# Optimization experiments

Hardware: AMD Instinct MI355X
Metric: run time of the kernel (lower is better)

Reference implementation:

```python
import jax, jax.numpy as jnp
import numpy as np

B, T, E, H, DEPTH = 128, 256, 512, 1024, 3


def setup_inputs() -> dict:
    key = jax.random.key(0)
    ks = jax.random.split(key, 9)
    s_e = 1.0 / np.sqrt(E)
    s_h = 1.0 / np.sqrt(H)
    return {
        "x": jax.random.normal(ks[0], (B, T, E), jnp.float32),
        "W_ih0": jax.random.normal(ks[1], (4 * H, E), jnp.float32) * s_e,
        "W_hh0": jax.random.normal(ks[2], (4 * H, H), jnp.float32) * s_h,
        "b_ih0": jax.random.normal(ks[3], (4 * H,), jnp.float32) * s_h,
        "b_hh0": jax.random.normal(ks[4], (4 * H,), jnp.float32) * s_h,
        "W_ih_r": jax.random.normal(ks[5], (DEPTH - 1, 4 * H, H), jnp.float32) * s_h,
        "W_hh_r": jax.random.normal(ks[6], (DEPTH - 1, 4 * H, H), jnp.float32) * s_h,
        "b_ih_r": jax.random.normal(ks[7], (DEPTH - 1, 4 * H), jnp.float32) * s_h,
        "b_hh_r": jax.random.normal(ks[8], (DEPTH - 1, 4 * H), jnp.float32) * s_h,
        "trainable": 1,
    }


def _lstm_cell(inp, h, c, Wih, Whh, bih, bhh):
    # torch.nn.LSTMCell: gates = inp @ Wih.T + bih + h @ Whh.T + bhh; order i,f,g,o
    gates = inp @ Wih.T + bih + h @ Whh.T + bhh
    i, f, g, o = jnp.split(gates, 4, axis=-1)
    c_new = jax.nn.sigmoid(f) * c + jax.nn.sigmoid(i) * jnp.tanh(g)
    h_new = jax.nn.sigmoid(o) * jnp.tanh(c_new)
    return h_new, c_new


def reference(x, W_ih0, W_hh0, b_ih0, b_hh0, W_ih_r, W_hh_r, b_ih_r, b_hh_r, trainable):
    b, _, _ = x.shape
    h_dim = W_hh0.shape[1]
    n_rest = W_ih_r.shape[0]
    zeros = jnp.zeros((b, h_dim), x.dtype)
    x_t = jnp.swapaxes(x, 0, 1)  # [T, B, E]

    def step(carry, xt):
        hs, cs = carry  # each [n_rest, B, H]
        # faithful bug: layer-0 state is never updated -> always zeros
        h, c = _lstm_cell(xt, zeros, zeros, W_ih0, W_hh0, b_ih0, b_hh0)
        new_h, new_c = [], []
        for l in range(n_rest):  # small fixed depth loop
            h, c = _lstm_cell(h, hs[l], cs[l], W_ih_r[l], W_hh_r[l], b_ih_r[l], b_hh_r[l])
            new_h.append(h)
            new_c.append(c)
        return (jnp.stack(new_h), jnp.stack(new_c)), h

    init = (jnp.zeros((n_rest, b, h_dim), x.dtype),
            jnp.zeros((n_rest, b, h_dim), x.dtype))
    _, out = jax.lax.scan(step, init, x_t)
    return out  # [T, B, H] == list of top-layer h per timestep
```

## Files before the change

### kernel.cpp

```cpp
#include <hip/hip_runtime.h>

static constexpr int Bc = 128;
static constexpr int Tc = 256;
static constexpr int Ec = 512;
static constexpr int Hc = 1024;
static constexpr int SLOT = Bc * Hc;

using bf16x8 = __attribute__((ext_vector_type(8))) short;
using f32x4  = __attribute__((ext_vector_type(4))) float;

__device__ __forceinline__ unsigned short f2bf(float f) {
  unsigned int u = __float_as_uint(f);
  u += 0x7FFFu + ((u >> 16) & 1u);
  return (unsigned short)(u >> 16);
}
__device__ __forceinline__ float sigm(float x) { return 1.0f / (1.0f + __expf(-x)); }
__device__ __forceinline__ float ftanh(float x) { return 1.0f - 2.0f / (__expf(2.0f * x) + 1.0f); }

#define MFMA16(A, Bf, C) __builtin_amdgcn_mfma_f32_16x16x32_bf16((A), (Bf), (C), 0, 0, 0)

__device__ __forceinline__ void poll_rlx(const int* p, int tgt) {
  while (__hip_atomic_load(p, __ATOMIC_RELAXED, __HIP_MEMORY_SCOPE_AGENT) < tgt)
    __builtin_amdgcn_s_sleep(1);
}
__device__ __forceinline__ void sig(int* p, int v) {
  __hip_atomic_store(p, v, __ATOMIC_RELAXED, __HIP_MEMORY_SCOPE_AGENT);
}
__device__ __forceinline__ void stg_c(unsigned short* p, unsigned short v) {
  __hip_atomic_store(p, v, __ATOMIC_RELAXED, __HIP_MEMORY_SCOPE_AGENT);
}
__device__ __forceinline__ int lds_acq(const int* p) {
  return __hip_atomic_load(p, __ATOMIC_ACQUIRE, __HIP_MEMORY_SCOPE_WORKGROUP);
}
__device__ __forceinline__ void lds_rel(int* p, int v) {
  __hip_atomic_store(p, v, __ATOMIC_RELEASE, __HIP_MEMORY_SCOPE_WORKGROUP);
}

__global__ void k_cvt_bf16(const float* __restrict__ src, unsigned short* __restrict__ dst, int n) {
  int i = (blockIdx.x * blockDim.x + threadIdx.x) * 4;
  if (i + 3 < n) {
    f32x4 v = *(const f32x4*)(src + i);
    *(ushort4*)(dst + i) = make_ushort4(f2bf(v[0]), f2bf(v[1]), f2bf(v[2]), f2bf(v[3]));
  }
}

__global__ void k_prep_small(const float* __restrict__ bih0, const float* __restrict__ bhh0,
                             float* __restrict__ b0s,
                             unsigned short* __restrict__ h2c,
                             int* __restrict__ f1, int* __restrict__ f2) {
  int i = blockIdx.x * blockDim.x + threadIdx.x;
  if (i < 4096) b0s[i] = bih0[i] + bhh0[i];
  h2c[i] = 0;
  if (i < 128 * 16) { f1[i] = 0; f2[i] = 0; }
}

__global__ __launch_bounds__(256, 1) void k_l0(
    const unsigned short* __restrict__ xb, const unsigned short* __restrict__ W0,
    const float* __restrict__ b0s, unsigned short* __restrict__ H0)
{
  __shared__ unsigned short Axs[64 * 128 * 8];
  const int tid = threadIdx.x;
  const int lane = tid & 63, wid = tid >> 6;
  const int bx = blockIdx.x;
  const int jbase = blockIdx.y * 64 + wid * 16;
  const int ri = lane & 15, kg = lane >> 4;

  for (int i = tid; i < 8192; i += 256) {
    const int row = i >> 6;
    const int chunk = i & 63;
    const int phys = chunk * 128 + (row ^ (chunk & 15));
    *(bf16x8*)(Axs + (size_t)phys * 8) =
        *(const bf16x8*)(xb + ((size_t)row * Tc + bx) * Ec + chunk * 8);
  }
  __syncthreads();

  const int j = jbase + ri;
  const float bi = b0s[j], bg = b0s[2 * Hc + j], bo = b0s[3 * Hc + j];
  const unsigned short* w0r = W0 + ((size_t)(0 * Hc + j)) * Ec + kg * 8;
  const unsigned short* w2r = W0 + ((size_t)(2 * Hc + j)) * Ec + kg * 8;
  const unsigned short* w3r = W0 + ((size_t)(3 * Hc + j)) * Ec + kg * 8;

  f32x4 ai[8], ag[8], ao[8];
#pragma unroll
  for (int u = 0; u < 8; ++u) { ai[u] = (f32x4){0,0,0,0}; ag[u] = (f32x4){0,0,0,0}; ao[u] = (f32x4){0,0,0,0}; }

#pragma unroll 4
  for (int kk = 0; kk < Ec / 32; ++kk) {
    bf16x8 wi = *(const bf16x8*)(w0r + kk * 32);
    bf16x8 wg = *(const bf16x8*)(w2r + kk * 32);
    bf16x8 wo = *(const bf16x8*)(w3r + kk * 32);
    const int ch = kk * 4 + kg;
#pragma unroll
    for (int u = 0; u < 8; ++u) {
      const int phys = ch * 128 + ((u * 16 + ri) ^ (ch & 15));
      bf16x8 a = *(const bf16x8*)(Axs + (size_t)phys * 8);
      ai[u] = MFMA16(a, wi, ai[u]);
      ag[u] = MFMA16(a, wg, ag[u]);
      ao[u] = MFMA16(a, wo, ao[u]);
    }
  }

  unsigned short* hb = H0 + (size_t)bx * SLOT + (size_t)(j >> 3) * 1024 + (j & 7);
#pragma unroll
  for (int u = 0; u < 8; ++u) {
#pragma unroll
    for (int q = 0; q < 4; ++q) {
      const int b = u * 16 + kg * 4 + q;
      float c = sigm(ai[u][q] + bi) * ftanh(ag[u][q] + bg);
      float h = sigm(ao[u][q] + bo) * ftanh(c);
      hb[(size_t)b * 8] = f2bf(h);
    }
  }
}

__global__ __launch_bounds__(512, 1) void k_rec(
    const unsigned short* H0,
    const float* __restrict__ Wih, const float* __restrict__ Whh,
    const float* __restrict__ bih, const float* __restrict__ bhh,
    unsigned short* h1c,
    unsigned short* h2c,
    int* f1, int* f2,
    float* out)
{
  __shared__ unsigned short Wlds[2 * 64 * 64 * 8];
  __shared__ float pbuf[4][4][64][4];
  __shared__ int flg[32];
  int* sF_   = flg + 0;
  int* sG_   = flg + 4;
  int* pollD = flg + 8;
  int* pollF = flg + 12;
  int* doneS = flg + 16;

  const int tid = threadIdx.x;
  const int lane = tid & 63, wid = tid >> 6;
  const int m = wid & 3;
  const bool gatedw = (wid >= 4);
  const int bid = blockIdx.x;
  const int layer = bid >> 7;
  const int w = bid & 127;
  const int j0 = w * 8;
  const int ri = lane & 15, kg = lane >> 4;

  if (tid < 32) flg[tid] = 0;

  const size_t lw = (size_t)layer * 4096 * 1024;
  for (int s = tid; s < 2 * 64 * 64; s += 512) {
    const int l   = s & 63;
    const int kkg = (s >> 6) & 63;
    const int t   = s >> 12;
    const int rr  = l & 15;
    const int gate = t * 2 + (rr >> 3);
    const int R = gate * 1024 + j0 + (rr & 7);
    const int k = kkg * 32 + (l >> 4) * 8;
    const float* src = (k < 1024) ? (Wih + lw + (size_t)R * 1024 + k)
                                  : (Whh + lw + (size_t)R * 1024 + (k - 1024));
    f32x4 v0 = *(const f32x4*)src;
    f32x4 v1 = *(const f32x4*)(src + 4);
    ushort4* d = (ushort4*)(Wlds + (size_t)s * 8);
    d[0] = make_ushort4(f2bf(v0[0]), f2bf(v0[1]), f2bf(v0[2]), f2bf(v0[3]));
    d[1] = make_ushort4(f2bf(v1[0]), f2bf(v1[1]), f2bf(v1[2]), f2bf(v1[3]));
  }

  const int jme = j0 + (ri & 7);
  const int g0 = (ri < 8) ? 0 : 1;
  const int g1 = (ri < 8) ? 2 : 3;
  const float bias0 = bih[layer * 4096 + g0 * 1024 + jme] + bhh[layer * 4096 + g0 * 1024 + jme];
  const float bias1 = bih[layer * 4096 + g1 * 1024 + jme] + bhh[layer * 4096 + g1 * 1024 + jme];

  float c0[4]  = {0.f, 0.f, 0.f, 0.f};
  float c1s[4] = {0.f, 0.f, 0.f, 0.f};

  const unsigned short* lds0 = Wlds + (size_t)lane * 8;
  const unsigned short* lds1 = Wlds + (size_t)64 * 64 * 8 + (size_t)lane * 8;
  const int abase = kg * 1024 + (m * 32 + ri) * 8;
  const bool lo = (ri < 8);

  f32x4 acc00, acc01, acc10, acc11;
#define ZERO4() { acc00 = (f32x4){0,0,0,0}; acc01 = (f32x4){0,0,0,0}; \
                  acc10 = (f32x4){0,0,0,0}; acc11 = (f32x4){0,0,0,0}; }
#define PLOAD()  { acc00 = *(const f32x4*)&pbuf[m][0][lane][0]; \
                   acc01 = *(const f32x4*)&pbuf[m][1][lane][0]; \
                   acc10 = *(const f32x4*)&pbuf[m][2][lane][0]; \
                   acc11 = *(const f32x4*)&pbuf[m][3][lane][0]; }
#define PWRITE() { *(f32x4*)&pbuf[m][0][lane][0] = acc00; \
                   *(f32x4*)&pbuf[m][1][lane][0] = acc01; \
                   *(f32x4*)&pbuf[m][2][lane][0] = acc10; \
                   *(f32x4*)&pbuf[m][3][lane][0] = acc11; }

#define HALF_MM4(Abase, LDSOFF)                                             \
  {                                                                         \
    const unsigned short* ap_ = (Abase) + abase;                            \
    _Pragma("unroll")                                                       \
    for (int kk = 0; kk < 32; ++kk) {                                       \
      bf16x8 b0 = *(const bf16x8*)(lds0 + (LDSOFF) + kk * 512);             \
      bf16x8 b1 = *(const bf16x8*)(lds1 + (LDSOFF) + kk * 512);             \
      bf16x8 vlo = *(const bf16x8*)(ap_ + kk * 4096);                       \
      bf16x8 vhi = *(const bf16x8*)(ap_ + kk * 4096 + 128);                 \
      acc00 = MFMA16(vlo, b0, acc00);                                       \
      acc01 = MFMA16(vlo, b1, acc01);                                       \
      acc10 = MFMA16(vhi, b0, acc10);                                       \
      acc11 = MFMA16(vhi, b1, acc11);                                       \
    }                                                                       \
  }

#define CELL4(accA, accB, cre, hnarr)                                       \
  _Pragma("unroll")                                                         \
  for (int q = 0; q < 4; ++q) {                                             \
    float x0 = accA[q] + bias0;                                             \
    float x1 = accB[q] + bias1;                                             \
    float p0 = __shfl_xor(x0, 8);                                           \
    float p1 = __shfl_xor(x1, 8);                                           \
    float gi = lo ? x0 : p0;                                                \
    float gf = lo ? p0 : x0;                                                \
    float gg = lo ? x1 : p1;                                                \
    float go = lo ? p1 : x1;                                                \
    float cn = sigm(gf) * cre[q] + sigm(gi) * ftanh(gg);                    \
    hnarr[q] = sigm(go) * ftanh(cn);                                        \
    cre[q] = cn;                                                            \
  }

#define GPOLL_BAR(farr, tgt, stamp)                                         \
  { if (lane < 32) poll_rlx((farr) + (m * 32 + lane) * 16, (tgt));          \
    if (lane == 0) lds_rel(&(stamp)[m], (tgt));                             \
    while (lds_acq(&(stamp)[0]) < (tgt) || lds_acq(&(stamp)[1]) < (tgt) ||  \
           lds_acq(&(stamp)[2]) < (tgt) || lds_acq(&(stamp)[3]) < (tgt)) {} }

  __syncthreads();

  if (layer == 0) {
    if (!gatedw) {
      ZERO4() HALF_MM4(H0, 0)
      for (int t = 0; t < Tc; ++t) {
        while (lds_acq(&sG_[m]) < t) {}
        PWRITE()
        if (lane == 0) lds_rel(&sF_[m], t + 1);
        if (t + 1 < Tc) { ZERO4() HALF_MM4(H0 + (size_t)(t + 1) * SLOT, 0) }
      }
    } else {
      for (int p = 0; p < Tc; ++p) {
        if (p >= 1) GPOLL_BAR(f1, p, pollD)
        while (lds_acq(&sF_[m]) < p + 1) {}
        PLOAD()
        if (lane == 0) lds_rel(&sG_[m], p + 1);
        if (p >= 1) HALF_MM4(h1c + (size_t)(p - 1) * SLOT, 32 * 512)
        float hn0[4], hn1[4];
        CELL4(acc00, acc01, c0, hn0)
        CELL4(acc10, acc11, c1s, hn1)
        if (lo) {
          unsigned short* hb = h1c + (size_t)p * SLOT + (size_t)w * 1024 + (ri & 7);
#pragma unroll
          for (int q = 0; q < 4; ++q) {
            const int r0 = m * 32 + kg * 4 + q;
            stg_c(hb + (size_t)r0 * 8, f2bf(hn0[q]));
            stg_c(hb + (size_t)(r0 + 16) * 8, f2bf(hn1[q]));
          }
        }
        __asm__ volatile("s_waitcnt vmcnt(0)" ::: "memory");
        if (lane == 0) lds_rel(&doneS[m], p + 1);
        if (m == 0) {
          while (lds_acq(&doneS[1]) < p + 1 || lds_acq(&doneS[2]) < p + 1 ||
                 lds_acq(&doneS[3]) < p + 1) {}
          if (lane == 0) sig(f1 + w * 16, p + 1);
        }
      }
    }
  } else {
    if (!gatedw) {
      GPOLL_BAR(f1, 1, pollF)
      ZERO4() HALF_MM4(h1c, 0)
      for (int t = 0; t < Tc; ++t) {
        while (lds_acq(&sG_[m]) < t) {}
        PWRITE()
        if (lane == 0) lds_rel(&sF_[m], t + 1);
        if (t + 1 < Tc) {
          GPOLL_BAR(f1, t + 2, pollF)
          ZERO4() HALF_MM4(h1c + (size_t)(t + 1) * SLOT, 0)
        }
      }
    } else {
      for (int s = 0; s < Tc; ++s) {
        if (s >= 1) GPOLL_BAR(f2, s, pollD)
        __builtin_amdgcn_fence(__ATOMIC_ACQUIRE, "agent");
        while (lds_acq(&sF_[m]) < s + 1) {}
        PLOAD()
        if (lane == 0) lds_rel(&sG_[m], s + 1);
        HALF_MM4(h2c + (size_t)((s - 1) & 3) * SLOT, 32 * 512)
        float hn0[4], hn1[4];
        CELL4(acc00, acc01, c0, hn0)
        CELL4(acc10, acc11, c1s, hn1)
        if (lo) {
          unsigned short* hb = h2c + (size_t)(s & 3) * SLOT + (size_t)w * 1024 + (ri & 7);
#pragma unroll
          for (int q = 0; q < 4; ++q) {
            const int r0 = m * 32 + kg * 4 + q;
            stg_c(hb + (size_t)r0 * 8, f2bf(hn0[q]));
            stg_c(hb + (size_t)(r0 + 16) * 8, f2bf(hn1[q]));
          }
        }
        __asm__ volatile("s_waitcnt vmcnt(0)" ::: "memory");
        if (lane == 0) lds_rel(&doneS[m], s + 1);
        if (m == 0) {
          while (lds_acq(&doneS[1]) < s + 1 || lds_acq(&doneS[2]) < s + 1 ||
                 lds_acq(&doneS[3]) < s + 1) {}
          if (lane == 0) sig(f2 + w * 16, s + 1);
        }
        if (lo) {
          float* po = out + (size_t)s * SLOT;
#pragma unroll
          for (int q = 0; q < 4; ++q) {
            const int r0 = m * 32 + kg * 4 + q;
            po[(size_t)r0 * Hc + jme] = hn0[q];
            po[(size_t)(r0 + 16) * Hc + jme] = hn1[q];
          }
        }
      }
    }
  }
}

extern "C" void kernel_launch(void* const* d_in, const int* in_sizes, int n_in,
                              void* d_out, int out_size, void* d_ws, size_t ws_size,
                              hipStream_t stream) {
  const float* x     = (const float*)d_in[0];
  const float* W_ih0 = (const float*)d_in[1];
  const float* b_ih0 = (const float*)d_in[3];
  const float* b_hh0 = (const float*)d_in[4];
  const float* W_ihr = (const float*)d_in[5];
  const float* W_hhr = (const float*)d_in[6];
  const float* b_ihr = (const float*)d_in[7];
  const float* b_hhr = (const float*)d_in[8];

  char* ws = (char*)d_ws;
  constexpr size_t H0_OFF  = 0;
  constexpr size_t H2B_OFF = H0_OFF + (size_t)Tc * SLOT * 2;
  constexpr size_t F1_OFF  = H2B_OFF + (size_t)4 * SLOT * 2;
  constexpr size_t F2_OFF  = F1_OFF + 128 * 16 * 4;

  unsigned short* H0  = (unsigned short*)(ws + H0_OFF);
  unsigned short* h2c = (unsigned short*)(ws + H2B_OFF);
  float* b0s = (float*)(ws + F2_OFF + 128 * 16 * 4);
  int* f1 = (int*)(ws + F1_OFF);
  int* f2 = (int*)(ws + F2_OFF);

  unsigned short* xb  = (unsigned short*)d_out;
  unsigned short* W0b = (unsigned short*)d_out + (size_t)Bc * Tc * Ec;
  unsigned short* h1c = (unsigned short*)d_out + (size_t)Tc * SLOT;
  float* out = (float*)d_out;

  int n0 = 4096 * 512;
  k_cvt_bf16<<<n0 / 1024, 256, 0, stream>>>(W_ih0, W0b, n0);
  int nx = Bc * Tc * Ec;
  k_cvt_bf16<<<nx / 1024, 256, 0, stream>>>(x, xb, nx);
  k_prep_small<<<2048, 256, 0, stream>>>(b_ih0, b_hh0, b0s, h2c, f1, f2);
  k_l0<<<dim3(Tc, 16), 256, 0, stream>>>(xb, W0b, b0s, H0);

  k_rec<<<dim3(256), dim3(512), 0, stream>>>(H0, W_ihr, W_hhr, b_ihr, b_hhr,
                                             h1c, h2c, f1, f2, out);
}
```

Baseline: 4.143 ms.

## Split recurrent matmul into per-group polls to overlap flag waits with MFMA

The recurrent-gate warps no longer wait at a full cross-block barrier for all 128 producer blocks before the recurrent matmul. Each step instead polls the producer flags in four groups of 32 without sleeping, and starts the MFMA slice for a group's K-range as soon as that group is ready. The layer-1 path drops the agent acquire fence and reads the hidden state with relaxed agent-scope atomic loads. This is meant to overlap synchronization latency with compute, at the cost of busy-spin polling and weaker memory-ordering guarantees on the layer-0 path, which keeps plain loads.

```diff
diff --git a/kernel.cpp b/kernel.cpp
--- a/kernel.cpp
+++ b/kernel.cpp
@@ -23,11 +23,20 @@
   while (__hip_atomic_load(p, __ATOMIC_RELAXED, __HIP_MEMORY_SCOPE_AGENT) < tgt)
     __builtin_amdgcn_s_sleep(1);
 }
+__device__ __forceinline__ void poll_fast(const int* p, int tgt) {
+  while (__hip_atomic_load(p, __ATOMIC_RELAXED, __HIP_MEMORY_SCOPE_AGENT) < tgt) {}
+}
 __device__ __forceinline__ void sig(int* p, int v) {
   __hip_atomic_store(p, v, __ATOMIC_RELAXED, __HIP_MEMORY_SCOPE_AGENT);
 }
 __device__ __forceinline__ void stg_c(unsigned short* p, unsigned short v) {
   __hip_atomic_store(p, v, __ATOMIC_RELAXED, __HIP_MEMORY_SCOPE_AGENT);
+}
+__device__ __forceinline__ bf16x8 ldg_c(const unsigned short* p) {
+  union { unsigned long long u[2]; bf16x8 v; } r;
+  r.u[0] = __hip_atomic_load((const unsigned long long*)p,       __ATOMIC_RELAXED, __HIP_MEMORY_SCOPE_AGENT);
+  r.u[1] = __hip_atomic_load((const unsigned long long*)(p + 4), __ATOMIC_RELAXED, __HIP_MEMORY_SCOPE_AGENT);
+  return r.v;
 }
 __device__ __forceinline__ int lds_acq(const int* p) {
   return __hip_atomic_load(p, __ATOMIC_ACQUIRE, __HIP_MEMORY_SCOPE_WORKGROUP);
@@ -127,7 +136,6 @@
   __shared__ int flg[32];
   int* sF_   = flg + 0;
   int* sG_   = flg + 4;
-  int* pollD = flg + 8;
   int* pollF = flg + 12;
   int* doneS = flg + 16;
 
@@ -187,15 +195,31 @@
                    *(f32x4*)&pbuf[m][2][lane][0] = acc10; \
                    *(f32x4*)&pbuf[m][3][lane][0] = acc11; }
 
-#define HALF_MM4(Abase, LDSOFF)                                             \
+#define HALF_MM4R(Abase, LDSOFF, K0, K1)                                    \
   {                                                                         \
     const unsigned short* ap_ = (Abase) + abase;                            \
     _Pragma("unroll")                                                       \
-    for (int kk = 0; kk < 32; ++kk) {                                       \
+    for (int kk = (K0); kk < (K1); ++kk) {                                  \
       bf16x8 b0 = *(const bf16x8*)(lds0 + (LDSOFF) + kk * 512);             \
       bf16x8 b1 = *(const bf16x8*)(lds1 + (LDSOFF) + kk * 512);             \
       bf16x8 vlo = *(const bf16x8*)(ap_ + kk * 4096);                       \
       bf16x8 vhi = *(const bf16x8*)(ap_ + kk * 4096 + 128);                 \
+      acc00 = MFMA16(vlo, b0, acc00);                                       \
+      acc01 = MFMA16(vlo, b1, acc01);                                       \
+      acc10 = MFMA16(vhi, b0, acc10);                                       \
+      acc11 = MFMA16(vhi, b1, acc11);                                       \
+    }                                                                       \
+  }
+
+#define HALF_MM4C(Abase, LDSOFF, K0, K1)                                    \
+  {                                                                         \
+    const unsigned short* ap_ = (Abase) + abase;                            \
+    _Pragma("unroll")                                                       \
+    for (int kk = (K0); kk < (K1); ++kk) {                                  \
+      bf16x8 b0 = *(const bf16x8*)(lds0 + (LDSOFF) + kk * 512);             \
+      bf16x8 b1 = *(const bf16x8*)(lds1 + (LDSOFF) + kk * 512);             \
+      bf16x8 vlo = ldg_c(ap_ + kk * 4096);                                  \
+      bf16x8 vhi = ldg_c(ap_ + kk * 4096 + 128);                            \
       acc00 = MFMA16(vlo, b0, acc00);                                       \
       acc01 = MFMA16(vlo, b1, acc01);                                       \
       acc10 = MFMA16(vhi, b0, acc10);                                       \
@@ -229,20 +253,26 @@
 
   if (layer == 0) {
     if (!gatedw) {
-      ZERO4() HALF_MM4(H0, 0)
+      ZERO4() HALF_MM4R(H0, 0, 0, 32)
       for (int t = 0; t < Tc; ++t) {
         while (lds_acq(&sG_[m]) < t) {}
         PWRITE()
         if (lane == 0) lds_rel(&sF_[m], t + 1);
-        if (t + 1 < Tc) { ZERO4() HALF_MM4(H0 + (size_t)(t + 1) * SLOT, 0) }
+        if (t + 1 < Tc) { ZERO4() HALF_MM4R(H0 + (size_t)(t + 1) * SLOT, 0, 0, 32) }
       }
     } else {
       for (int p = 0; p < Tc; ++p) {
-        if (p >= 1) GPOLL_BAR(f1, p, pollD)
         while (lds_acq(&sF_[m]) < p + 1) {}
         PLOAD()
         if (lane == 0) lds_rel(&sG_[m], p + 1);
-        if (p >= 1) HALF_MM4(h1c + (size_t)(p - 1) * SLOT, 32 * 512)
+        if (p >= 1) {
+          const unsigned short* gb = h1c + (size_t)(p - 1) * SLOT;
+#pragma unroll
+          for (int g = 0; g < 4; ++g) {
+            if (lane < 32) poll_fast(f1 + (g * 32 + lane) * 16, p);
+            HALF_MM4R(gb, 32 * 512, 8 * g, 8 * g + 8)
+          }
+        }
         float hn0[4], hn1[4];
         CELL4(acc00, acc01, c0, hn0)
         CELL4(acc10, acc11, c1s, hn1)
@@ -267,24 +297,29 @@
   } else {
     if (!gatedw) {
       GPOLL_BAR(f1, 1, pollF)
-      ZERO4() HALF_MM4(h1c, 0)
+      ZERO4() HALF_MM4R(h1c, 0, 0, 32)
       for (int t = 0; t < Tc; ++t) {
         while (lds_acq(&sG_[m]) < t) {}
         PWRITE()
         if (lane == 0) lds_rel(&sF_[m], t + 1);
         if (t + 1 < Tc) {
           GPOLL_BAR(f1, t + 2, pollF)
-          ZERO4() HALF_MM4(h1c + (size_t)(t + 1) * SLOT, 0)
+          ZERO4() HALF_MM4R(h1c + (size_t)(t + 1) * SLOT, 0, 0, 32)
         }
       }
     } else {
       for (int s = 0; s < Tc; ++s) {
-        if (s >= 1) GPOLL_BAR(f2, s, pollD)
-        __builtin_amdgcn_fence(__ATOMIC_ACQUIRE, "agent");
         while (lds_acq(&sF_[m]) < s + 1) {}
         PLOAD()
         if (lane == 0) lds_rel(&sG_[m], s + 1);
-        HALF_MM4(h2c + (size_t)((s - 1) & 3) * SLOT, 32 * 512)
+        {
+          const unsigned short* gb = h2c + (size_t)((s - 1) & 3) * SLOT;
+#pragma unroll
+          for (int g = 0; g < 4; ++g) {
+            if (s >= 1 && lane < 32) poll_fast(f2 + (g * 32 + lane) * 16, s);
+            HALF_MM4C(gb, 32 * 512, 8 * g, 8 * g + 8)
+          }
+        }
         float hn0[4], hn1[4];
         CELL4(acc00, acc01, c0, hn0)
         CELL4(acc10, acc11, c1s, hn1)
```

Result: faster. 3.818 ms, median of 2 (-7.8%).
